# Performance work log

Hardware: AMD Instinct MI355X
Metric: run time of the kernel (lower is better)

Reference implementation:

```python
import jax, jax.numpy as jnp
import numpy as np

N_EMBED = 384
BLOCK_SIZE = 256
HEAD_SIZE = 64
B, T = 256, 256


def setup_inputs() -> dict:
    key = jax.random.key(0)
    k1, k2, k3, k4 = jax.random.split(key, 4)
    x = jax.random.normal(k1, (B, T, N_EMBED), dtype=jnp.float32)
    Wq = jax.random.normal(k2, (N_EMBED, HEAD_SIZE), dtype=jnp.float32) * (N_EMBED ** -0.5)
    Wk = jax.random.normal(k3, (N_EMBED, HEAD_SIZE), dtype=jnp.float32) * (N_EMBED ** -0.5)
    Wv = jax.random.normal(k4, (N_EMBED, HEAD_SIZE), dtype=jnp.float32) * (N_EMBED ** -0.5)
    return {"x": x, "Wq": Wq, "Wk": Wk, "Wv": Wv}


def reference(x, Wq, Wk, Wv):
    Bb, Tt, C = x.shape
    q = jnp.einsum("btc,ch->bth", x, Wq)
    k = jnp.einsum("btc,ch->bth", x, Wk)
    v = jnp.einsum("btc,ch->bth", x, Wv)
    # NOTE: original scales by C**-0.5 where C = n_embed (384), not head_size
    scale = jnp.asarray(C, x.dtype) ** -0.5
    wei = jnp.einsum("bqh,bkh->bqk", q, k) * scale  # [B, T, T]
    causal = jnp.tril(jnp.ones((Tt, Tt), dtype=bool))
    wei = jnp.where(causal, wei, -jnp.inf)
    wei = jax.nn.softmax(wei, axis=-1)
    out = jnp.einsum("bqk,bkh->bqh", wei, v)
    return out
```

## Files before the change

kernel.cpp:

```cpp
#include <hip/hip_runtime.h>
#include <hip/hip_bf16.h>
#include <math.h>

#define BB   256
#define TT   256
#define CIN  384
#define HS   64
#define BT   (BB*TT)

#define QSCL ((float)(0.051031036307982884 * 1.4426950408889634))

typedef __attribute__((ext_vector_type(8))) short short8;
typedef __attribute__((ext_vector_type(4))) float floatx4;

__device__ inline short bf16bits(float f) {
    union { __hip_bfloat16 h; short s; } u;
    u.h = __float2bfloat16(f);
    return u.s;
}

__device__ inline short8 cvt8(const float4& f0, const float4& f1) {
    union { __hip_bfloat162 h[4]; short8 s8; } u;
    u.h[0] = __float22bfloat162_rn(make_float2(f0.x, f0.y));
    u.h[1] = __float22bfloat162_rn(make_float2(f0.z, f0.w));
    u.h[2] = __float22bfloat162_rn(make_float2(f1.x, f1.y));
    u.h[3] = __float22bfloat162_rn(make_float2(f1.z, f1.w));
    return u.s8;
}

__global__ __launch_bounds__(256) void prep_wtp(
    const float* __restrict__ Wq, const float* __restrict__ Wk,
    const float* __restrict__ Wv, short* __restrict__ WtP)
{
    const int idx  = blockIdx.x * 256 + threadIdx.x;
    const int j    = idx & 7;
    const int quad = (idx >> 3) & 3;
    const int l15  = (idx >> 5) & 15;
    int X          = idx >> 9;
    const int nt   = X % 6;  X /= 6;
    const int ks   = X & 1;  X >>= 1;
    const int s    = X % 6;  X /= 6;
    const int wn   = X;

    const int n  = wn * 96 + nt * 16 + l15;
    const int kk = s * 64 + ks * 32 + quad * 8 + j;
    const float* W = (n < 64) ? Wq : (n < 128) ? Wk : Wv;
    WtP[idx] = bf16bits(W[kk * 64 + (n & 63)]);
}

__global__ __launch_bounds__(512) void fused_head(
    const float* __restrict__ x, const short* __restrict__ WtP,
    float* __restrict__ out)
{
    __shared__ short smem[58880];

    const int tid  = threadIdx.x;
    const int b    = blockIdx.x;
    const int lane = tid & 63;
    const int w    = tid >> 6;
    const int wm   = w >> 1;
    const int wn   = w & 1;
    const int l15  = lane & 15;
    const int quad = lane >> 4;
    const int kq   = quad * 8;
    const int crow = quad * 4;

    const float* xb = x + (size_t)b * 256 * 384;
    const int laneoff = l15 * 32 + quad * 8;

    floatx4 acc[4][6] = {};

#pragma unroll
    for (int i = 0; i < 4; ++i) {
        const int c   = i * 512 + tid;
        const int row = c >> 3;
        const int ch  = (c & 7) * 8;
        const float* p = xb + (size_t)row * 384 + ch;
        *(short8*)&smem[row * 72 + ch] = cvt8(*(const float4*)p, *(const float4*)(p + 4));
    }
    float4 pf[2][4][2];
#pragma unroll
    for (int i = 0; i < 4; ++i) {
        const int c   = i * 512 + tid;
        const int row = c >> 3;
        const int ch  = (c & 7) * 8;
        const float* p = xb + (size_t)row * 384 + 64 + ch;
        pf[1][i][0] = *(const float4*)p;
        pf[1][i][1] = *(const float4*)(p + 4);
    }
    __syncthreads();

#pragma unroll
    for (int s = 0; s < 6; ++s) {
        short* cur = smem + (s & 1) * 18432;
        short* nxt = smem + ((s & 1) ^ 1) * 18432;

        if (s < 4) {
#pragma unroll
            for (int i = 0; i < 4; ++i) {
                const int c   = i * 512 + tid;
                const int row = c >> 3;
                const int ch  = (c & 7) * 8;
                const float* p = xb + (size_t)row * 384 + (s + 2) * 64 + ch;
                pf[s & 1][i][0] = *(const float4*)p;
                pf[s & 1][i][1] = *(const float4*)(p + 4);
            }
        }

        short8 bf[2][6];
#pragma unroll
        for (int ks = 0; ks < 2; ++ks)
#pragma unroll
            for (int nt = 0; nt < 6; ++nt)
                bf[ks][nt] = *(const short8*)
                    &WtP[((((wn * 6 + s) * 2 + ks) * 6 + nt) << 9) + laneoff];

#pragma unroll
        for (int ks = 0; ks < 2; ++ks) {
            short8 af[4];
#pragma unroll
            for (int mt = 0; mt < 4; ++mt)
                af[mt] = *(const short8*)&cur[(wm * 64 + mt * 16 + l15) * 72 + ks * 32 + kq];
#pragma unroll
            for (int mt = 0; mt < 4; ++mt)
#pragma unroll
                for (int nt = 0; nt < 6; ++nt)
                    acc[mt][nt] = __builtin_amdgcn_mfma_f32_16x16x32_bf16(
                        af[mt], bf[ks][nt], acc[mt][nt], 0, 0, 0);
        }

        if (s < 5) {
#pragma unroll
            for (int i = 0; i < 4; ++i) {
                const int c   = i * 512 + tid;
                const int row = c >> 3;
                const int ch  = (c & 7) * 8;
                *(short8*)&nxt[row * 72 + ch] =
                    cvt8(pf[(s + 1) & 1][i][0], pf[(s + 1) & 1][i][1]);
            }
        }
        __syncthreads();
    }

    short* q_lds = smem;
    short* k_lds = smem + 18432;
    short* vt    = smem + 36864;
    short* Ps    = smem + 53760;

    const int nbase = wn * 96;
#pragma unroll
    for (int nt = 0; nt < 6; ++nt) {
        const int n = nbase + nt * 16 + l15;
#pragma unroll
        for (int mt = 0; mt < 4; ++mt) {
#pragma unroll
            for (int r = 0; r < 4; ++r) {
                const int m = wm * 64 + mt * 16 + crow + r;
                const float av = acc[mt][nt][r];
                if (n < 64)       q_lds[m * 72 + n]          = bf16bits(av * QSCL);
                else if (n < 128) k_lds[m * 72 + (n - 64)]   = bf16bits(av);
                else              vt[(n - 128) * 264 + m]    = bf16bits(av);
            }
        }
    }
    __syncthreads();

#pragma unroll
    for (int g = 0; g < 2; ++g) {
        const int r0 = w * 32 + g * 16;

        short8 aq0, aq1;
        aq0 = *(const short8*)&q_lds[(r0 + l15) * 72 + kq];
        aq1 = *(const short8*)&q_lds[(r0 + l15) * 72 + 32 + kq];

        float lsum[4] = {0.f, 0.f, 0.f, 0.f};
        floatx4 O[4] = {};

        const int nch = (r0 + 47) >> 5;
        for (int c = 0; c < nch; ++c) {
            const int cb = c * 32;

            floatx4 st[2];
#pragma unroll
            for (int t = 0; t < 2; ++t) {
                const short8 b0 = *(const short8*)&k_lds[(cb + t * 16 + l15) * 72 + kq];
                const short8 b1 = *(const short8*)&k_lds[(cb + t * 16 + l15) * 72 + 32 + kq];
                floatx4 z = {};
                z = __builtin_amdgcn_mfma_f32_16x16x32_bf16(aq0, b0, z, 0, 0, 0);
                z = __builtin_amdgcn_mfma_f32_16x16x32_bf16(aq1, b1, z, 0, 0, 0);
                st[t] = z;
            }

#pragma unroll
            for (int t = 0; t < 2; ++t)
#pragma unroll
                for (int r = 0; r < 4; ++r) {
                    const int key  = cb + t * 16 + l15;
                    const int qrow = r0 + crow + r;
                    float p = __builtin_amdgcn_exp2f(st[t][r]);
                    p = (key <= qrow) ? p : 0.f;
                    lsum[r] += p;
                    Ps[w * 640 + (crow + r) * 40 + t * 16 + l15] = bf16bits(p);
                }

            asm volatile("s_waitcnt lgkmcnt(0)" ::: "memory");

            const short8 pa = *(const short8*)&Ps[w * 640 + l15 * 40 + kq];
#pragma unroll
            for (int n = 0; n < 4; ++n) {
                const short8 bv = *(const short8*)&vt[(n * 16 + l15) * 264 + cb + kq];
                O[n] = __builtin_amdgcn_mfma_f32_16x16x32_bf16(pa, bv, O[n], 0, 0, 0);
            }
        }

#pragma unroll
        for (int off = 1; off < 16; off <<= 1)
#pragma unroll
            for (int r = 0; r < 4; ++r)
                lsum[r] += __shfl_xor(lsum[r], off, 16);

        float inv[4];
#pragma unroll
        for (int r = 0; r < 4; ++r) inv[r] = 1.f / lsum[r];
#pragma unroll
        for (int n = 0; n < 4; ++n)
#pragma unroll
            for (int r = 0; r < 4; ++r)
                out[(size_t)(b * 256 + r0 + crow + r) * 64 + n * 16 + l15] = O[n][r] * inv[r];
    }
}

extern "C" void kernel_launch(void* const* d_in, const int* in_sizes, int n_in,
                              void* d_out, int out_size, void* d_ws, size_t ws_size,
                              hipStream_t stream)
{
    const float* x  = (const float*)d_in[0];
    const float* Wq = (const float*)d_in[1];
    const float* Wk = (const float*)d_in[2];
    const float* Wv = (const float*)d_in[3];
    float* out = (float*)d_out;

    short* WtP = (short*)d_ws;

    prep_wtp<<<(192 * 384) / 256, 256, 0, stream>>>(Wq, Wk, Wv, WtP);
    fused_head<<<BB, 512, 0, stream>>>(x, WtP, out);
}
```

Measured before the change: 171.8 us.

## Load x directly into MFMA registers per wave and balance causal row groups

The QKV projection no longer stages x through double-buffered LDS with block-wide barriers. Each wave now loads its own 32 rows of x straight from global memory into registers in the MFMA operand layout, converts them to bf16 in place, and computes all 192 output columns, reading the weight fragments from global memory. The attention phase also pairs row group w with group 15-w so every wave gets a similar amount of causal work. In exchange, each wave rereads the full weight matrix from global or L2, the global x loads are less coalesced, and register pressure from 24 accumulators is higher.

```diff
diff --git a/kernel.cpp b/kernel.cpp
--- a/kernel.cpp
+++ b/kernel.cpp
@@ -58,8 +58,6 @@
     const int b    = blockIdx.x;
     const int lane = tid & 63;
     const int w    = tid >> 6;
-    const int wm   = w >> 1;
-    const int wn   = w & 1;
     const int l15  = lane & 15;
     const int quad = lane >> 4;
     const int kq   = quad * 8;
@@ -68,78 +66,60 @@
     const float* xb = x + (size_t)b * 256 * 384;
     const int laneoff = l15 * 32 + quad * 8;
 
-    floatx4 acc[4][6] = {};
-
-#pragma unroll
-    for (int i = 0; i < 4; ++i) {
-        const int c   = i * 512 + tid;
-        const int row = c >> 3;
-        const int ch  = (c & 7) * 8;
-        const float* p = xb + (size_t)row * 384 + ch;
-        *(short8*)&smem[row * 72 + ch] = cvt8(*(const float4*)p, *(const float4*)(p + 4));
+    floatx4 acc[2][12] = {};
+
+    const float* xr0 = xb + (size_t)(w * 32 +      l15) * 384 + kq;
+    const float* xr1 = xb + (size_t)(w * 32 + 16 + l15) * 384 + kq;
+
+    float4 cur[2][2][2];
+#pragma unroll
+    for (int ks = 0; ks < 2; ++ks) {
+        cur[0][ks][0] = *(const float4*)(xr0 + ks * 32);
+        cur[0][ks][1] = *(const float4*)(xr0 + ks * 32 + 4);
+        cur[1][ks][0] = *(const float4*)(xr1 + ks * 32);
+        cur[1][ks][1] = *(const float4*)(xr1 + ks * 32 + 4);
     }
-    float4 pf[2][4][2];
-#pragma unroll
-    for (int i = 0; i < 4; ++i) {
-        const int c   = i * 512 + tid;
-        const int row = c >> 3;
-        const int ch  = (c & 7) * 8;
-        const float* p = xb + (size_t)row * 384 + 64 + ch;
-        pf[1][i][0] = *(const float4*)p;
-        pf[1][i][1] = *(const float4*)(p + 4);
-    }
-    __syncthreads();
 
 #pragma unroll
     for (int s = 0; s < 6; ++s) {
-        short* cur = smem + (s & 1) * 18432;
-        short* nxt = smem + ((s & 1) ^ 1) * 18432;
-
-        if (s < 4) {
-#pragma unroll
-            for (int i = 0; i < 4; ++i) {
-                const int c   = i * 512 + tid;
-                const int row = c >> 3;
-                const int ch  = (c & 7) * 8;
-                const float* p = xb + (size_t)row * 384 + (s + 2) * 64 + ch;
-                pf[s & 1][i][0] = *(const float4*)p;
-                pf[s & 1][i][1] = *(const float4*)(p + 4);
-            }
-        }
-
-        short8 bf[2][6];
-#pragma unroll
-        for (int ks = 0; ks < 2; ++ks)
-#pragma unroll
-            for (int nt = 0; nt < 6; ++nt)
-                bf[ks][nt] = *(const short8*)
-                    &WtP[((((wn * 6 + s) * 2 + ks) * 6 + nt) << 9) + laneoff];
+        float4 nxt[2][2][2];
+        if (s < 5) {
+#pragma unroll
+            for (int ks = 0; ks < 2; ++ks) {
+                nxt[0][ks][0] = *(const float4*)(xr0 + (s + 1) * 64 + ks * 32);
+                nxt[0][ks][1] = *(const float4*)(xr0 + (s + 1) * 64 + ks * 32 + 4);
+                nxt[1][ks][0] = *(const float4*)(xr1 + (s + 1) * 64 + ks * 32);
+                nxt[1][ks][1] = *(const float4*)(xr1 + (s + 1) * 64 + ks * 32 + 4);
+            }
+        }
 
 #pragma unroll
         for (int ks = 0; ks < 2; ++ks) {
-            short8 af[4];
-#pragma unroll
-            for (int mt = 0; mt < 4; ++mt)
-                af[mt] = *(const short8*)&cur[(wm * 64 + mt * 16 + l15) * 72 + ks * 32 + kq];
-#pragma unroll
-            for (int mt = 0; mt < 4; ++mt)
-#pragma unroll
-                for (int nt = 0; nt < 6; ++nt)
-                    acc[mt][nt] = __builtin_amdgcn_mfma_f32_16x16x32_bf16(
-                        af[mt], bf[ks][nt], acc[mt][nt], 0, 0, 0);
+            short8 af0 = cvt8(cur[0][ks][0], cur[0][ks][1]);
+            short8 af1 = cvt8(cur[1][ks][0], cur[1][ks][1]);
+#pragma unroll
+            for (int h = 0; h < 2; ++h)
+#pragma unroll
+                for (int nt = 0; nt < 6; ++nt) {
+                    const short8 bf = *(const short8*)
+                        &WtP[((((h * 6 + s) * 2 + ks) * 6 + nt) << 9) + laneoff];
+                    const int j = h * 6 + nt;
+                    acc[0][j] = __builtin_amdgcn_mfma_f32_16x16x32_bf16(
+                        af0, bf, acc[0][j], 0, 0, 0);
+                    acc[1][j] = __builtin_amdgcn_mfma_f32_16x16x32_bf16(
+                        af1, bf, acc[1][j], 0, 0, 0);
+                }
         }
 
         if (s < 5) {
 #pragma unroll
-            for (int i = 0; i < 4; ++i) {
-                const int c   = i * 512 + tid;
-                const int row = c >> 3;
-                const int ch  = (c & 7) * 8;
-                *(short8*)&nxt[row * 72 + ch] =
-                    cvt8(pf[(s + 1) & 1][i][0], pf[(s + 1) & 1][i][1]);
-            }
-        }
-        __syncthreads();
+            for (int mt = 0; mt < 2; ++mt)
+#pragma unroll
+                for (int ks = 0; ks < 2; ++ks) {
+                    cur[mt][ks][0] = nxt[mt][ks][0];
+                    cur[mt][ks][1] = nxt[mt][ks][1];
+                }
+        }
     }
 
     short* q_lds = smem;
@@ -147,27 +127,26 @@
     short* vt    = smem + 36864;
     short* Ps    = smem + 53760;
 
-    const int nbase = wn * 96;
-#pragma unroll
-    for (int nt = 0; nt < 6; ++nt) {
-        const int n = nbase + nt * 16 + l15;
-#pragma unroll
-        for (int mt = 0; mt < 4; ++mt) {
+#pragma unroll
+    for (int mt = 0; mt < 2; ++mt)
+#pragma unroll
+        for (int j = 0; j < 12; ++j) {
+            const int n = j * 16 + l15;
 #pragma unroll
             for (int r = 0; r < 4; ++r) {
-                const int m = wm * 64 + mt * 16 + crow + r;
-                const float av = acc[mt][nt][r];
-                if (n < 64)       q_lds[m * 72 + n]          = bf16bits(av * QSCL);
-                else if (n < 128) k_lds[m * 72 + (n - 64)]   = bf16bits(av);
-                else              vt[(n - 128) * 264 + m]    = bf16bits(av);
-            }
-        }
-    }
+                const int m = w * 32 + mt * 16 + crow + r;
+                const float av = acc[mt][j][r];
+                if (j < 4)      q_lds[m * 72 + n]          = bf16bits(av * QSCL);
+                else if (j < 8) k_lds[m * 72 + (n - 64)]   = bf16bits(av);
+                else            vt[(n - 128) * 264 + m]    = bf16bits(av);
+            }
+        }
     __syncthreads();
 
 #pragma unroll
     for (int g = 0; g < 2; ++g) {
-        const int r0 = w * 32 + g * 16;
+        const int grp = g ? (15 - w) : w;
+        const int r0  = grp * 16;
 
         short8 aq0, aq1;
         aq0 = *(const short8*)&q_lds[(r0 + l15) * 72 + kq];
```

New measurement: 179.8 us. 1.05x slower.
